# Kernel optimization log

Measured on AMD Instinct MI355X. Metric: run time of the kernel, lower is better.

Reference implementation:

```python
import jax, jax.numpy as jnp
import numpy as np

B, Q, K, D, H = 8, 200, 16384, 256, 8
ALIGN_K, CROSS_K, FF = 96, 1024, 1024
DH = D // H

def _l2norm(x):
    n = jnp.linalg.norm(x, axis=-1, keepdims=True)
    return x / jnp.maximum(n, 1e-6)

def _layernorm(x, g, b):
    mu = jnp.mean(x, axis=-1, keepdims=True)
    v = jnp.var(x, axis=-1, keepdims=True)
    return (x - mu) / jnp.sqrt(v + 1e-5) * g + b

def _mha(xq, xk, xv, in_w, in_b, out_w, out_b, bias=None):
    # torch nn.MultiheadAttention (batch_first, eval mode)
    wq, wk, wv = jnp.split(in_w, 3, axis=0)
    bq, bk, bv = jnp.split(in_b, 3, axis=0)
    def heads(x, w, bb):
        y = x @ w.T + bb
        return y.reshape(x.shape[0], x.shape[1], H, DH).transpose(0, 2, 1, 3)
    qh, kh, vh = heads(xq, wq, bq), heads(xk, wk, bk), heads(xv, wv, bv)
    s = jnp.einsum('bhqd,bhkd->bhqk', qh, kh) / (DH ** 0.5)
    if bias is not None:
        s = s + bias
    a = jax.nn.softmax(s, axis=-1)
    o = jnp.einsum('bhqk,bhkd->bhqd', a, vh).transpose(0, 2, 1, 3).reshape(xq.shape[0], xq.shape[1], D)
    return o @ out_w.T + out_b

def setup_inputs():
    key = jax.random.key(0)
    ks = jax.random.split(key, 40)
    r = lambda i, sh, s=1.0: jax.random.normal(ks[i], sh, jnp.float32) * s
    W = 0.02
    return dict(
        q=r(0, (B, Q, D)), q_pos=r(1, (B, Q, D)), memory=r(2, (B, K, D)),
        cross_attn_bias=r(3, (B, Q, K), 0.1),
        align_wq=r(4, (D, D), W), align_wm=r(5, (D, D), W),
        gate_w1=r(6, (D, 2 * D), W), gate_b1=jnp.zeros((D,), jnp.float32),
        gate_w2=r(7, (D, D), W), gate_b2=jnp.zeros((D,), jnp.float32),
        cross_wq=r(8, (D, D), W), cross_wm=r(9, (D, D), W),
        sa_in_w=r(10, (3 * D, D), W), sa_in_b=jnp.zeros((3 * D,), jnp.float32),
        sa_out_w=r(11, (D, D), W), sa_out_b=jnp.zeros((D,), jnp.float32),
        ca_in_w=r(12, (3 * D, D), W), ca_in_b=jnp.zeros((3 * D,), jnp.float32),
        ca_out_w=r(13, (D, D), W), ca_out_b=jnp.zeros((D,), jnp.float32),
        ffn_w1=r(14, (FF, D), W), ffn_b1=jnp.zeros((FF,), jnp.float32),
        ffn_w2=r(15, (D, FF), W), ffn_b2=jnp.zeros((D,), jnp.float32),
        n1_g=jnp.ones((D,), jnp.float32), n1_b=jnp.zeros((D,), jnp.float32),
        n2_g=jnp.ones((D,), jnp.float32), n2_b=jnp.zeros((D,), jnp.float32),
        n3_g=jnp.ones((D,), jnp.float32), n3_b=jnp.zeros((D,), jnp.float32))

def reference(q, q_pos, memory, cross_attn_bias, align_wq, align_wm, gate_w1, gate_b1,
              gate_w2, gate_b2, cross_wq, cross_wm, sa_in_w, sa_in_b, sa_out_w, sa_out_b,
              ca_in_w, ca_in_b, ca_out_w, ca_out_b, ffn_w1, ffn_b1, ffn_w2, ffn_b2,
              n1_g, n1_b, n2_g, n2_b, n3_g, n3_b):
    # --- query-memory align: proj+normalize+sim+topk+gather+softmax+weighted-sum ---
    qn = _l2norm(q @ align_wq.T)
    mn = _l2norm(memory @ align_wm.T)
    sim = jnp.einsum('bqd,bkd->bqk', qn, mn)            # [B,Q,K]
    vals, idx = jax.lax.top_k(sim, ALIGN_K)             # [B,Q,ALIGN_K]
    selected = jax.vmap(lambda m, i: m[i])(memory, idx) # [B,Q,ALIGN_K,D]
    w = jax.nn.softmax(vals, axis=-1)
    aligned = jnp.einsum('bqk,bqkd->bqd', w, selected)
    h = jax.nn.gelu(jnp.concatenate([q, aligned], axis=-1) @ gate_w1.T + gate_b1, approximate=False)
    gate = jax.nn.sigmoid(h @ gate_w2.T + gate_b2)
    qx = q + gate * aligned
    # --- self attention ---
    qk = qx + q_pos
    q2 = _mha(qk, qk, qx, sa_in_w, sa_in_b, sa_out_w, sa_out_b)
    qx = _layernorm(qx + q2, n1_g, n1_b)
    # --- cross-memory sparsify (topk over K) ---
    qn2 = _l2norm(qx @ cross_wq.T)
    mn2 = _l2norm(memory @ cross_wm.T)
    sim2 = jnp.einsum('bqd,bkd->bqk', qn2, mn2)
    importance = sim2.max(axis=1)                       # [B,K]
    _, kidx = jax.lax.top_k(importance, CROSS_K)        # [B,CROSS_K]
    mem_sel = jax.vmap(lambda m, i: m[i])(memory, kidx) # [B,CROSS_K,D]
    bias_sel = jnp.take_along_axis(
        cross_attn_bias, jnp.broadcast_to(kidx[:, None, :], (B, Q, CROSS_K)), axis=2)
    bias4 = jnp.broadcast_to(bias_sel[:, None], (B, H, Q, CROSS_K))
    q2 = _mha(qx + q_pos, mem_sel, mem_sel, ca_in_w, ca_in_b, ca_out_w, ca_out_b, bias4)
    qx = _layernorm(qx + q2, n2_g, n2_b)
    # --- FFN ---
    f = jax.nn.gelu(qx @ ffn_w1.T + ffn_b1, approximate=False) @ ffn_w2.T + ffn_b2
    return _layernorm(qx + f, n3_g, n3_b)
```

## Files before the change

kernel.cpp:

```cpp
#include <hip/hip_runtime.h>
#include <hip/hip_bf16.h>
#include <math.h>

#define B_ 8
#define Q_ 200
#define K_ 16384
#define D_ 256
#define H_ 8
#define DH_ 32
#define ALIGNK_ 96
#define CROSSK_ 1024
#define FF_ 1024
#define BQ_ (B_*Q_)
#define BK_ (B_*K_)

typedef unsigned short u16;
typedef short bf16x8 __attribute__((ext_vector_type(8)));
typedef float f32x4 __attribute__((ext_vector_type(4)));

__device__ __forceinline__ float b2f(u16 u){ return __uint_as_float(((unsigned)u)<<16); }
__device__ __forceinline__ u16 f2b(float f){
  unsigned x = __float_as_uint(f);
  unsigned r = x + 0x7FFFu + ((x>>16)&1u);
  return (u16)(r>>16);
}
__device__ __forceinline__ unsigned p2u(float lo, float hi){
  return (unsigned)f2b(lo) | ((unsigned)f2b(hi)<<16);
}
__device__ __forceinline__ uint4 pk8(float4 a, float4 b){
  return make_uint4(p2u(a.x,a.y), p2u(a.z,a.w), p2u(b.x,b.y), p2u(b.z,b.w));
}
__device__ __forceinline__ unsigned fkey(float f){ unsigned b=__float_as_uint(f); return (b&0x80000000u)? ~b : (b|0x80000000u); }
__device__ __forceinline__ float funkey(unsigned k){ unsigned b=(k&0x80000000u)? (k^0x80000000u) : ~k; return __uint_as_float(b); }
__device__ __forceinline__ float gelu_f(float x){ return 0.5f*x*(1.0f+erff(x*0.70710678118654752f)); }
__device__ __forceinline__ float sigmoid_f(float x){ return 1.0f/(1.0f+__expf(-x)); }

struct GArgs {
  const void* A; const void* B; const float* bias;
  float* Cf; u16* Cb; unsigned* amax;
  const int* gather;
  long lda, ldb, ldc;
  long sA, sB, sC, sAmax, sGather;
  int M, N, K, act;
};

template<int AF32, int BF32>
__global__ __launch_bounds__(256) void gemm_bt(GArgs g)
{
  const int tid = threadIdx.x;
  const int bz = blockIdx.z;
  const int m0 = blockIdx.y*64, n0 = blockIdx.x*64;
  const int lane = tid & 63, wave = tid >> 6;
  const int wr = wave >> 1, wc = wave & 1;
  __shared__ __align__(16) u16 As[64][72];
  __shared__ __align__(16) u16 Bs[64][72];
  f32x4 acc[2][2] = {};

  const int lrow = tid>>2;
  const int lk = (tid&3)*16;
  int ar = m0 + lrow; if (ar > g.M-1) ar = g.M-1;
  if (g.gather) ar = g.gather[(long)bz*g.sGather + ar];
  int br = n0 + lrow; if (br > g.N-1) br = g.N-1;
  long aoff = (long)bz*g.sA + (long)ar*g.lda + lk;
  long boff = (long)bz*g.sB + (long)br*g.ldb + lk;

  const int nk = g.K >> 6;
  for (int kt=0; kt<nk; ++kt){
    uint4 wa0, wa1, wb0, wb1;
    if (AF32){
      const float* p = (const float*)g.A + aoff;
      float4 f0 = *(const float4*)(p+0);
      float4 f1 = *(const float4*)(p+4);
      float4 f2v= *(const float4*)(p+8);
      float4 f3 = *(const float4*)(p+12);
      wa0 = pk8(f0,f1); wa1 = pk8(f2v,f3);
    } else {
      const u16* p = (const u16*)g.A + aoff;
      wa0 = *(const uint4*)p; wa1 = *(const uint4*)(p+8);
    }
    if (BF32){
      const float* p = (const float*)g.B + boff;
      float4 f0 = *(const float4*)(p+0);
      float4 f1 = *(const float4*)(p+4);
      float4 f2v= *(const float4*)(p+8);
      float4 f3 = *(const float4*)(p+12);
      wb0 = pk8(f0,f1); wb1 = pk8(f2v,f3);
    } else {
      const u16* p = (const u16*)g.B + boff;
      wb0 = *(const uint4*)p; wb1 = *(const uint4*)(p+8);
    }
    aoff += 64; boff += 64;
    __syncthreads();
    *(uint4*)&As[lrow][lk]   = wa0; *(uint4*)&As[lrow][lk+8] = wa1;
    *(uint4*)&Bs[lrow][lk]   = wb0; *(uint4*)&Bs[lrow][lk+8] = wb1;
    __syncthreads();
    #pragma unroll
    for (int kk=0; kk<2; ++kk){
      const int ko = kk*32 + (lane>>4)*8;
      bf16x8 af0 = *(const bf16x8*)&As[wr*32      + (lane&15)][ko];
      bf16x8 af1 = *(const bf16x8*)&As[wr*32 + 16 + (lane&15)][ko];
      bf16x8 bf0 = *(const bf16x8*)&Bs[wc*32      + (lane&15)][ko];
      bf16x8 bf1 = *(const bf16x8*)&Bs[wc*32 + 16 + (lane&15)][ko];
      acc[0][0] = __builtin_amdgcn_mfma_f32_16x16x32_bf16(af0, bf0, acc[0][0], 0,0,0);
      acc[0][1] = __builtin_amdgcn_mfma_f32_16x16x32_bf16(af0, bf1, acc[0][1], 0,0,0);
      acc[1][0] = __builtin_amdgcn_mfma_f32_16x16x32_bf16(af1, bf0, acc[1][0], 0,0,0);
      acc[1][1] = __builtin_amdgcn_mfma_f32_16x16x32_bf16(af1, bf1, acc[1][1], 0,0,0);
    }
  }

  if (g.amax){
    #pragma unroll
    for (int j=0;j<2;j++){
      float mx = -3.0e38f;
      #pragma unroll
      for (int i=0;i<2;i++)
        #pragma unroll
        for (int r=0;r<4;r++) mx = fmaxf(mx, acc[i][j][r]);
      mx = fmaxf(mx, __shfl_xor(mx, 16));
      mx = fmaxf(mx, __shfl_xor(mx, 32));
      if ((lane>>4)==0){
        int n = n0 + wc*32 + j*16 + (lane&15);
        if (n < g.N) atomicMax(&g.amax[(long)bz*g.sAmax + n], fkey(mx));
      }
    }
    return;
  }

  #pragma unroll
  for (int i=0;i<2;i++)
  #pragma unroll
  for (int j=0;j<2;j++)
  #pragma unroll
  for (int r=0;r<4;r++){
    int m = m0 + wr*32 + i*16 + (lane>>4)*4 + r;
    int n = n0 + wc*32 + j*16 + (lane&15);
    if (m < g.M && n < g.N){
      float v = acc[i][j][r];
      if (g.bias) v += g.bias[n];
      if (g.act==1) v = gelu_f(v);
      else if (g.act==2) v = sigmoid_f(v);
      long ci = (long)bz*g.sC + (long)m*g.ldc + n;
      if (g.Cf) g.Cf[ci] = v; else g.Cb[ci] = f2b(v);
    }
  }
}

__global__ void w2b_kernel(const float* w, u16* wb, int n)
{
  int i = (blockIdx.x*256 + threadIdx.x)*8;
  if (i < n){
    float4 a = *(const float4*)(w+i), b = *(const float4*)(w+i+4);
    *(uint4*)(wb+i) = pk8(a,b);
  }
}

template<int AF32>
__global__ __launch_bounds__(256) void proj_l2norm(
    const void* Ain, long lda, const u16* Wb, u16* outp, int R)
{
  __shared__ __align__(16) u16 As[64][72];
  __shared__ __align__(16) u16 Bs[64][72];
  const int tid = threadIdx.x;
  const int m0 = blockIdx.x*64;
  const int lane = tid & 63, wave = tid >> 6;
  f32x4 acc[4][4] = {};

  const int lrow = tid>>2, lk = (tid&3)*16;
  int ar = m0 + lrow; if (ar > R-1) ar = R-1;

  for (int kt=0; kt<4; ++kt){
    uint4 wa0, wa1;
    if (AF32){
      const float* p = (const float*)Ain + (long)ar*lda + kt*64 + lk;
      wa0 = pk8(*(const float4*)(p+0), *(const float4*)(p+4));
      wa1 = pk8(*(const float4*)(p+8), *(const float4*)(p+12));
    } else {
      const u16* p = (const u16*)Ain + (long)ar*lda + kt*64 + lk;
      wa0 = *(const uint4*)p; wa1 = *(const uint4*)(p+8);
    }
    #pragma unroll
    for (int nc=0; nc<4; ++nc){
      const u16* wp = Wb + (long)(nc*64 + lrow)*256 + kt*64 + lk;
      uint4 wb0 = *(const uint4*)wp;
      uint4 wb1 = *(const uint4*)(wp+8);
      __syncthreads();
      if (nc==0){ *(uint4*)&As[lrow][lk] = wa0; *(uint4*)&As[lrow][lk+8] = wa1; }
      *(uint4*)&Bs[lrow][lk] = wb0; *(uint4*)&Bs[lrow][lk+8] = wb1;
      __syncthreads();
      #pragma unroll
      for (int kk=0; kk<2; ++kk){
        const int ko = kk*32 + (lane>>4)*8;
        bf16x8 af = *(const bf16x8*)&As[wave*16 + (lane&15)][ko];
        #pragma unroll
        for (int j=0; j<4; j++){
          bf16x8 bfr = *(const bf16x8*)&Bs[j*16 + (lane&15)][ko];
          acc[nc][j] = __builtin_amdgcn_mfma_f32_16x16x32_bf16(af, bfr, acc[nc][j], 0,0,0);
        }
      }
    }
  }

  #pragma unroll
  for (int r=0;r<4;r++){
    float ssq = 0.f;
    #pragma unroll
    for (int nc=0;nc<4;nc++)
      #pragma unroll
      for (int j=0;j<4;j++) ssq += acc[nc][j][r]*acc[nc][j][r];
    ssq += __shfl_xor(ssq,1); ssq += __shfl_xor(ssq,2);
    ssq += __shfl_xor(ssq,4); ssq += __shfl_xor(ssq,8);
    float inv = 1.0f/fmaxf(sqrtf(ssq), 1e-6f);
    int row = m0 + wave*16 + (lane>>4)*4 + r;
    if (row < R){
      u16* op = outp + (long)row*256 + (lane&15);
      #pragma unroll
      for (int nc=0;nc<4;nc++)
        #pragma unroll
        for (int j=0;j<4;j++) op[nc*64 + j*16] = f2b(acc[nc][j][r]*inv);
    }
  }
}

__global__ __launch_bounds__(256) void topk_kernel(const float* inF, const unsigned* inK,
    long in_stride, int RANK, float* out_val, int* out_idx)
{
  __shared__ int red[2][4];
  __shared__ int redt[4];
  __shared__ int poss;
  int row = blockIdx.x, tid = threadIdx.x;
  unsigned kr[64];
  if (inF){
    const float4* p = (const float4*)(inF + (long)row*in_stride);
    #pragma unroll
    for (int jj=0;jj<16;jj++){
      float4 v = p[tid + jj*256];
      kr[jj*4+0]=fkey(v.x); kr[jj*4+1]=fkey(v.y); kr[jj*4+2]=fkey(v.z); kr[jj*4+3]=fkey(v.w);
    }
  } else {
    const uint4* p = (const uint4*)(inK + (long)row*in_stride);
    #pragma unroll
    for (int jj=0;jj<16;jj++){
      uint4 v = p[tid + jj*256];
      kr[jj*4+0]=v.x; kr[jj*4+1]=v.y; kr[jj*4+2]=v.z; kr[jj*4+3]=v.w;
    }
  }
  if (tid==0) poss = 0;

  unsigned u = 0; bool exact = false; int pp = 0;
  for (int bit=31; bit>=0; --bit){
    unsigned cand = u | (1u<<bit);
    int c = 0;
    #pragma unroll
    for (int j=0;j<64;j++) c += (kr[j] >= cand) ? 1 : 0;
    #pragma unroll
    for (int off=32; off; off>>=1) c += __shfl_down(c, off);
    if ((tid&63)==0) red[pp][tid>>6] = c;
    __syncthreads();
    c = red[pp][0]+red[pp][1]+red[pp][2]+red[pp][3];
    pp ^= 1;
    if (c >= RANK){
      u = cand;
      if (c == RANK){ exact = true; break; }
    }
  }

  int t = 0;
  if (!exact){
    int cgt = 0;
    #pragma unroll
    for (int j=0;j<64;j++) cgt += (kr[j] > u) ? 1 : 0;
    #pragma unroll
    for (int off=32; off; off>>=1) cgt += __shfl_down(cgt, off);
    __syncthreads();
    if ((tid&63)==0) redt[tid>>6] = cgt;
    __syncthreads();
    cgt = redt[0]+redt[1]+redt[2]+redt[3];
    int Req = RANK - cgt;
    for (int bit=13; bit>=0; --bit){
      int cand = t | (1<<bit);
      int c = 0;
      #pragma unroll
      for (int j=0;j<64;j++){
        int e = (tid<<2) + (j&3) + ((j>>2)<<10);
        c += (kr[j]==u && e < cand) ? 1 : 0;
      }
      #pragma unroll
      for (int off=32; off; off>>=1) c += __shfl_down(c, off);
      __syncthreads();
      if ((tid&63)==0) redt[tid>>6] = c;
      __syncthreads();
      c = redt[0]+redt[1]+redt[2]+redt[3];
      if (c < Req) t = cand;
    }
  }
  __syncthreads();
  #pragma unroll
  for (int j=0;j<64;j++){
    int e = (tid<<2) + (j&3) + ((j>>2)<<10);
    unsigned kk = kr[j];
    bool win = exact ? (kk >= u) : (kk > u || (kk == u && e <= t));
    if (win){
      int p2 = atomicAdd(&poss, 1);
      out_val[(long)row*RANK + p2] = funkey(kk);
      out_idx[(long)row*RANK + p2] = e;
    }
  }
}

__global__ __launch_bounds__(256) void align_combine(const float* vals, const int* idx,
    const float* memory, float* alignedv)
{
  __shared__ float w[96];
  __shared__ int id[96];
  __shared__ float reds[2];
  int row = blockIdx.x, tid = threadIdx.x;
  int b = row / 200;
  if (tid < 96){ w[tid] = vals[(long)row*96 + tid]; id[tid] = idx[(long)row*96 + tid]; }
  __syncthreads();
  if (tid < 64){
    float a = w[tid];
    float bb2 = (tid < 32) ? w[64+tid] : -3e38f;
    float m = fmaxf(a, bb2);
    #pragma unroll
    for (int off=32; off; off>>=1) m = fmaxf(m, __shfl_xor(m, off));
    if (tid==0) reds[0] = m;
  }
  __syncthreads();
  float m = reds[0];
  if (tid < 96) w[tid] = __expf(w[tid]-m);
  __syncthreads();
  if (tid < 64){
    float a = w[tid] + ((tid<32)? w[64+tid] : 0.f);
    #pragma unroll
    for (int off=32; off; off>>=1) a += __shfl_xor(a, off);
    if (tid==0) reds[1] = a;
  }
  __syncthreads();
  float invs = 1.0f/reds[1];
  float acc = 0.f;
  const float* mb = memory + (long)b*K_*D_;
  for (int k=0;k<96;k++) acc += w[k] * mb[(long)id[k]*D_ + tid];
  alignedv[(long)row*256 + tid] = acc*invs;
}

__global__ void make_cat(const float* q, const float* alignedv, u16* cat)
{
  int row = blockIdx.x, tid = threadIdx.x;
  long i = (long)row*256 + tid;
  cat[(long)row*512 + tid]       = f2b(q[i]);
  cat[(long)row*512 + 256 + tid] = f2b(alignedv[i]);
}

__global__ void combine_gate(const float* q, const float* q_pos, const float* alignedv,
    const float* gate, float* qx, u16* qx_b, u16* qk_b)
{
  int row = blockIdx.x, tid = threadIdx.x;
  long i = (long)row*256 + tid;
  float v = q[i] + gate[i]*alignedv[i];
  qx[i] = v;
  qx_b[i] = f2b(v);
  qk_b[i] = f2b(v + q_pos[i]);
}

__global__ __launch_bounds__(256) void add_ln(const float* x, const float* y,
    const float* g, const float* bb, const float* q_pos,
    float* out_f, u16* out_b, u16* out_pos_b)
{
  __shared__ float red[8];
  int row = blockIdx.x, tid = threadIdx.x;
  long i = (long)row*256 + tid;
  float t = fminf(fmaxf(x[i] + y[i], -1e6f), 1e6f);
  float s1 = t, s2 = t*t;
  #pragma unroll
  for (int off=32; off; off>>=1){ s1 += __shfl_down(s1,off); s2 += __shfl_down(s2,off); }
  if ((tid&63)==0){ red[(tid>>6)*2] = s1; red[(tid>>6)*2+1] = s2; }
  __syncthreads();
  s1 = red[0]+red[2]+red[4]+red[6];
  s2 = red[1]+red[3]+red[5]+red[7];
  float mu = s1 * (1.0f/256.0f);
  float var = fmaxf(s2 * (1.0f/256.0f) - mu*mu, 0.f);
  float rstd = rsqrtf(var + 1e-5f);
  float v = (t-mu)*rstd*g[tid] + bb[tid];
  if (out_f) out_f[i] = v;
  if (out_b) out_b[i] = f2b(v);
  if (out_pos_b) out_pos_b[i] = f2b(v + q_pos[i]);
}

__global__ void fill_u32(unsigned* p, unsigned val, int n)
{ int i = blockIdx.x*256 + threadIdx.x; if (i<n) p[i] = val; }

__global__ __launch_bounds__(256) void bias_gather2(const float* cbias, const int* kidx,
    float* biasTq)
{
  int qq = blockIdx.x, b = blockIdx.y;
  const float* src = cbias + ((long)b*200+qq)*(long)K_;
  float* dst = biasTq + ((long)b*200+qq)*CROSSK_;
  const int* kp = kidx + b*CROSSK_;
  for (int j=threadIdx.x; j<CROSSK_; j+=256) dst[j] = src[kp[j]];
}

__global__ __launch_bounds__(256) void qk_score(
    const u16* Qb, int q_stride, const u16* KVb, int kv_stride, int k_off,
    int Lk, int Jpad, const float* biasTq, float* S, float scale)
{
  __shared__ __align__(16) u16 Qs[64][40];
  __shared__ __align__(16) u16 Ks[64][40];
  const int bh = blockIdx.z, b = bh>>3, h = bh&7;
  const int q0 = blockIdx.y*64, j0 = blockIdx.x*64;
  const int tid = threadIdx.x, lane = tid&63, w = tid>>6;
  {
    int row = tid>>2, c8 = (tid&3)*8;
    int qr = q0+row; if (qr>199) qr=199;
    *(uint4*)&Qs[row][c8] = *(const uint4*)(Qb + (long)(b*200+qr)*q_stride + h*32 + c8);
    int j = j0+row;
    uint4 kv = make_uint4(0,0,0,0);
    if (j < Lk) kv = *(const uint4*)(KVb + (long)(b*Lk+j)*kv_stride + k_off + c8);
    *(uint4*)&Ks[row][c8] = kv;
  }
  __syncthreads();
  bf16x8 af = *(const bf16x8*)&Qs[w*16 + (lane&15)][(lane>>4)*8];
  f32x4 acc[4];
  #pragma unroll
  for (int jj=0;jj<4;jj++){
    f32x4 zz = {};
    bf16x8 bfr = *(const bf16x8*)&Ks[jj*16 + (lane&15)][(lane>>4)*8];
    acc[jj] = __builtin_amdgcn_mfma_f32_16x16x32_bf16(af, bfr, zz, 0,0,0);
  }
  #pragma unroll
  for (int jj=0;jj<4;jj++)
  #pragma unroll
  for (int r=0;r<4;r++){
    int q = q0 + w*16 + (lane>>4)*4 + r;
    int j = j0 + jj*16 + (lane&15);
    if (q < 200){
      float s = acc[jj][r]*scale;
      if (biasTq) s += biasTq[((long)(b*200+q))*Jpad + j];
      if (j >= Lk) s = -3e38f;
      S[((long)bh*200 + q)*Jpad + j] = s;
    }
  }
}

template<int JP>
__global__ __launch_bounds__(256) void softmax_p(const float* S, u16* P)
{
  __shared__ float red[8];
  const long base = (long)blockIdx.x * JP;
  const int tid = threadIdx.x;
  constexpr int PER = JP/256;
  float v[PER];
  float m = -3e38f;
  #pragma unroll
  for (int i=0;i<PER;i++){ v[i] = S[base + tid + i*256]; m = fmaxf(m, v[i]); }
  #pragma unroll
  for (int off=32; off; off>>=1) m = fmaxf(m, __shfl_xor(m, off));
  if ((tid&63)==0) red[tid>>6] = m;
  __syncthreads();
  m = fmaxf(fmaxf(red[0],red[1]), fmaxf(red[2],red[3]));
  float s = 0.f;
  #pragma unroll
  for (int i=0;i<PER;i++){ v[i] = __expf(v[i]-m); s += v[i]; }
  #pragma unroll
  for (int off=32; off; off>>=1) s += __shfl_xor(s, off);
  if ((tid&63)==0) red[4+(tid>>6)] = s;
  __syncthreads();
  s = red[4]+red[5]+red[6]+red[7];
  float inv = 1.0f/s;
  #pragma unroll
  for (int i=0;i<PER;i++) P[base + tid + i*256] = f2b(v[i]*inv);
}

__global__ __launch_bounds__(256) void pv_kernel(
    const u16* P, int Jpad, const u16* KVb, int kv_stride, int v_off, int Lk,
    u16* outp)
{
  __shared__ __align__(16) u16 Vt[32][72];
  const int bh = blockIdx.y, b = bh>>3, h = bh&7;
  const int q0 = blockIdx.x*64;
  const int tid = threadIdx.x, lane = tid&63, w = tid>>6;
  f32x4 acc[2] = {};
  int qa = q0 + w*16 + (lane&15); if (qa>199) qa=199;
  const u16* Prow = P + ((long)bh*200 + qa)*Jpad;
  const int jrow = lane;
  const int d0 = w*8;

  for (int j0=0; j0<Jpad; j0+=64){
    int j = j0 + jrow;
    uint4 vv = make_uint4(0,0,0,0);
    if (j < Lk) vv = *(const uint4*)(KVb + (long)(b*Lk+j)*kv_stride + v_off + d0);
    __syncthreads();
    Vt[d0+0][jrow] = (u16)(vv.x&0xffffu); Vt[d0+1][jrow] = (u16)(vv.x>>16);
    Vt[d0+2][jrow] = (u16)(vv.y&0xffffu); Vt[d0+3][jrow] = (u16)(vv.y>>16);
    Vt[d0+4][jrow] = (u16)(vv.z&0xffffu); Vt[d0+5][jrow] = (u16)(vv.z>>16);
    Vt[d0+6][jrow] = (u16)(vv.w&0xffffu); Vt[d0+7][jrow] = (u16)(vv.w>>16);
    __syncthreads();
    #pragma unroll
    for (int ks=0; ks<2; ks++){
      bf16x8 af = *(const bf16x8*)(Prow + j0 + ks*32 + (lane>>4)*8);
      #pragma unroll
      for (int dd=0; dd<2; dd++){
        bf16x8 bfr = *(const bf16x8*)&Vt[dd*16 + (lane&15)][ks*32 + (lane>>4)*8];
        acc[dd] = __builtin_amdgcn_mfma_f32_16x16x32_bf16(af, bfr, acc[dd], 0,0,0);
      }
    }
  }
  #pragma unroll
  for (int dd=0; dd<2; dd++)
  #pragma unroll
  for (int r=0; r<4; r++){
    int qq = q0 + w*16 + (lane>>4)*4 + r;
    if (qq < 200)
      outp[((long)(b*200+qq))*256 + h*32 + dd*16 + (lane&15)] = f2b(acc[dd][r]);
  }
}

__global__ __launch_bounds__(256) void attn_kernel(
    const u16* Qb, int q_stride,
    const u16* KVb, int kv_stride, int k_off, int v_off, int Lk,
    const float* biasTq,
    int nsplit, int chunk,
    float* opart, float* mlpart, float scale)
{
  __shared__ float Ks[64][36];
  __shared__ float Vs[64][36];
  const int b = blockIdx.z, h = blockIdx.y;
  const int split = blockIdx.x % nsplit;
  const int q0 = (blockIdx.x / nsplit) * 64;
  const int tid = threadIdx.x;
  const int cg = tid & 3, r = tid >> 2;
  const int kbeg = split*chunk;
  int kend = kbeg + chunk; if (kend > Lk) kend = Lk;

  int qr = q0 + r; if (qr > 199) qr = 199;
  float qreg[32];
  {
    const u16* qp = Qb + (long)(b*200+qr)*q_stride + h*32;
    #pragma unroll
    for (int w=0; w<4; w++){
      uint4 u = *(const uint4*)(qp + w*8);
      qreg[w*8+0]=b2f((u16)(u.x&0xffffu))*scale; qreg[w*8+1]=b2f((u16)(u.x>>16))*scale;
      qreg[w*8+2]=b2f((u16)(u.y&0xffffu))*scale; qreg[w*8+3]=b2f((u16)(u.y>>16))*scale;
      qreg[w*8+4]=b2f((u16)(u.z&0xffffu))*scale; qreg[w*8+5]=b2f((u16)(u.z>>16))*scale;
      qreg[w*8+6]=b2f((u16)(u.w&0xffffu))*scale; qreg[w*8+7]=b2f((u16)(u.w>>16))*scale;
    }
  }
  const float* bT = biasTq ? biasTq + ((long)(b*200+qr))*CROSSK_ : nullptr;

  float o32[32];
  #pragma unroll
  for (int i=0;i<32;i++) o32[i]=0.f;
  float mrun = -3e38f, lrun = 0.f;

  const int srow = tid>>2, sc8 = (tid&3)*8;
  for (int j0=kbeg; j0<kend; j0+=64){
    int kr = j0 + srow; if (kr > kend-1) kr = kend-1;
    const long base = (long)(b*Lk + kr)*kv_stride;
    uint4 ku = *(const uint4*)(KVb + base + k_off + sc8);
    uint4 vu = *(const uint4*)(KVb + base + v_off + sc8);
    __syncthreads();
    {
      float4 f0, f1;
      f0.x=b2f((u16)(ku.x&0xffffu)); f0.y=b2f((u16)(ku.x>>16)); f0.z=b2f((u16)(ku.y&0xffffu)); f0.w=b2f((u16)(ku.y>>16));
      f1.x=b2f((u16)(ku.z&0xffffu)); f1.y=b2f((u16)(ku.z>>16)); f1.z=b2f((u16)(ku.w&0xffffu)); f1.w=b2f((u16)(ku.w>>16));
      *(float4*)&Ks[srow][sc8] = f0; *(float4*)&Ks[srow][sc8+4] = f1;
      f0.x=b2f((u16)(vu.x&0xffffu)); f0.y=b2f((u16)(vu.x>>16)); f0.z=b2f((u16)(vu.y&0xffffu)); f0.w=b2f((u16)(vu.y>>16));
      f1.x=b2f((u16)(vu.z&0xffffu)); f1.y=b2f((u16)(vu.z>>16)); f1.z=b2f((u16)(vu.w&0xffffu)); f1.w=b2f((u16)(vu.w>>16));
      *(float4*)&Vs[srow][sc8] = f0; *(float4*)&Vs[srow][sc8+4] = f1;
    }
    __syncthreads();

    float sv[16];
    float mloc = -3e38f;
    #pragma unroll
    for (int jj=0;jj<16;jj++){
      const int c = cg + jj*4;
      const float4* kp = (const float4*)&Ks[c][0];
      float a = 0.f;
      #pragma unroll
      for (int dq=0;dq<8;dq++){
        float4 kv = kp[dq];
        a += qreg[dq*4+0]*kv.x + qreg[dq*4+1]*kv.y + qreg[dq*4+2]*kv.z + qreg[dq*4+3]*kv.w;
      }
      if (bT) a += bT[j0 + c];
      if (j0 + c >= kend) a = -3e38f;
      sv[jj] = a; mloc = fmaxf(mloc, a);
    }
    mloc = fmaxf(mloc, __shfl_xor(mloc,1));
    mloc = fmaxf(mloc, __shfl_xor(mloc,2));
    const float mnew = fmaxf(mrun, mloc);
    const float alpha = __expf(mrun - mnew);
    float lloc = 0.f;
    #pragma unroll
    for (int jj=0;jj<16;jj++){
      float p = (j0 + cg + jj*4 >= kend) ? 0.f : __expf(sv[jj]-mnew);
      sv[jj] = p; lloc += p;
    }
    lloc += __shfl_xor(lloc,1);
    lloc += __shfl_xor(lloc,2);
    lrun = lrun*alpha + lloc;
    #pragma unroll
    for (int i=0;i<32;i++) o32[i] *= alpha;
    #pragma unroll
    for (int jj=0;jj<16;jj++){
      const int c = cg + jj*4;
      const float p = sv[jj];
      const float4* vp = (const float4*)&Vs[c][0];
      #pragma unroll
      for (int dq=0;dq<8;dq++){
        float4 v = vp[dq];
        o32[dq*4+0] += p*v.x; o32[dq*4+1] += p*v.y; o32[dq*4+2] += p*v.z; o32[dq*4+3] += p*v.w;
      }
    }
    mrun = mnew;
  }

  #pragma unroll
  for (int d=0;d<32;d++){
    float v = o32[d];
    v += __shfl_xor(v,1);
    v += __shfl_xor(v,2);
    o32[d] = v;
  }
  if (q0 + r < 200){
    const long pbase = (((long)(b*H_+h)*nsplit + split)*200) + (q0 + r);
    float* op = opart + pbase*32;
    #pragma unroll
    for (int i=0;i<8;i++) op[cg*8+i] = o32[cg*8+i];
    if (cg==0){ mlpart[pbase*2] = mrun; mlpart[pbase*2+1] = lrun; }
  }
}

__global__ __launch_bounds__(256) void attn_combine(const float* opart, const float* mlpart,
    int nsplit, u16* outp)
{
  int row = blockIdx.x;
  int b = row/200, qi = row%200;
  int tid = threadIdx.x;
  int h = tid>>5, d = tid&31;
  const long base = ((long)(b*H_+h)*nsplit)*200 + qi;
  float M = -3e38f;
  for (int s=0;s<nsplit;s++) M = fmaxf(M, mlpart[(base + (long)s*200)*2]);
  float L = 0.f, acc = 0.f;
  for (int s=0;s<nsplit;s++){
    const long ix = base + (long)s*200;
    float w = __expf(mlpart[ix*2] - M);
    L   += mlpart[ix*2+1]*w;
    acc += opart[ix*32 + d]*w;
  }
  outp[(long)row*256 + h*32 + d] = f2b(acc / fmaxf(L, 1e-30f));
}

extern "C" void kernel_launch(void* const* d_in, const int* in_sizes, int n_in,
                              void* d_out, int out_size, void* d_ws, size_t ws_size,
                              hipStream_t stream)
{
  const float* q        = (const float*)d_in[0];
  const float* q_pos    = (const float*)d_in[1];
  const float* memory   = (const float*)d_in[2];
  const float* cbias    = (const float*)d_in[3];
  const float* align_wq = (const float*)d_in[4];
  const float* align_wm = (const float*)d_in[5];
  const float* gate_w1  = (const float*)d_in[6];
  const float* gate_b1  = (const float*)d_in[7];
  const float* gate_w2  = (const float*)d_in[8];
  const float* gate_b2  = (const float*)d_in[9];
  const float* cross_wq = (const float*)d_in[10];
  const float* cross_wm = (const float*)d_in[11];
  const float* sa_in_w  = (const float*)d_in[12];
  const float* sa_in_b  = (const float*)d_in[13];
  const float* sa_out_w = (const float*)d_in[14];
  const float* sa_out_b = (const float*)d_in[15];
  const float* ca_in_w  = (const float*)d_in[16];
  const float* ca_in_b  = (const float*)d_in[17];
  const float* ca_out_w = (const float*)d_in[18];
  const float* ca_out_b = (const float*)d_in[19];
  const float* ffn_w1   = (const float*)d_in[20];
  const float* ffn_b1   = (const float*)d_in[21];
  const float* ffn_w2   = (const float*)d_in[22];
  const float* ffn_b2   = (const float*)d_in[23];
  const float* n1_g = (const float*)d_in[24];
  const float* n1_b = (const float*)d_in[25];
  const float* n2_g = (const float*)d_in[26];
  const float* n2_b = (const float*)d_in[27];
  const float* n3_g = (const float*)d_in[28];
  const float* n3_b = (const float*)d_in[29];
  float* out = (float*)d_out;

  char* wsb = (char*)d_ws;
  size_t off = 0;
  auto alloc = [&](size_t bytes)->char*{
    char* p = wsb + off; off = (off + bytes + 255) & ~(size_t)255; return p;
  };
  const int NSPLIT = 4;
  u16*    qn_bf   = (u16*)   alloc((size_t)BQ_*D_*2);
  float*  vals96  = (float*) alloc((size_t)BQ_*96*4);
  int*    idx96   = (int*)   alloc((size_t)BQ_*96*4);
  float*  alignedv= (float*) alloc((size_t)BQ_*D_*4);
  u16*    cat_bf  = (u16*)   alloc((size_t)BQ_*512*2);
  u16*    h_bf    = (u16*)   alloc((size_t)BQ_*D_*2);
  float*  gatebuf = (float*) alloc((size_t)BQ_*D_*4);
  float*  qx      = (float*) alloc((size_t)BQ_*D_*4);
  u16*    qx_bf   = (u16*)   alloc((size_t)BQ_*D_*2);
  u16*    qk_bf   = (u16*)   alloc((size_t)BQ_*D_*2);
  u16*    qpos2_bf= (u16*)   alloc((size_t)BQ_*D_*2);
  u16*    qkv_bf  = (u16*)   alloc((size_t)BQ_*768*2);
  u16*    attO_bf = (u16*)   alloc((size_t)BQ_*D_*2);
  float*  q2      = (float*) alloc((size_t)BQ_*D_*4);
  unsigned* imp   = (unsigned*)alloc((size_t)B_*K_*4);
  int*    kidx    = (int*)   alloc((size_t)B_*CROSSK_*4);
  u16*    cq_bf   = (u16*)   alloc((size_t)BQ_*D_*2);
  u16*    f1_bf   = (u16*)   alloc((size_t)BQ_*FF_*2);
  float*  f2buf   = (float*) alloc((size_t)BQ_*D_*4);
  float*  opart   = (float*) alloc((size_t)B_*H_*NSPLIT*200*32*4);
  float*  mlpart  = (float*) alloc((size_t)B_*H_*NSPLIT*200*2*4);
  float*  biasTq  = (float*) alloc((size_t)B_*Q_*CROSSK_*4);
  u16*    wb_alwq = (u16*)   alloc((size_t)D_*D_*2);
  u16*    wb_alwm = (u16*)   alloc((size_t)D_*D_*2);
  u16*    wb_crwq = (u16*)   alloc((size_t)D_*D_*2);
  u16*    wb_crwm = (u16*)   alloc((size_t)D_*D_*2);

  const size_t kv_bytes   = (size_t)B_*CROSSK_*512*2;
  const size_t mn_full    = (size_t)BK_*D_*2;
  const size_t mn_small   = (size_t)K_*D_*2;
  const size_t sim_full   = (size_t)BQ_*K_*4;
  size_t remain = (ws_size > off) ? ws_size - off : 0;
  bool fullws = remain >= mn_full + sim_full + (1u<<20);
  size_t mn_bytes = fullws ? mn_full : (mn_small > kv_bytes ? mn_small : kv_bytes);
  int simRows;
  if (fullws) simRows = BQ_;
  else {
    size_t left = (remain > mn_bytes + (1u<<18)) ? remain - mn_bytes - (1u<<18) : 0;
    long r = (long)(left / ((size_t)K_*4));
    simRows = (int)(r < 8 ? 8 : (r > Q_ ? Q_ : r));
  }
  u16*   mn_bf  = (u16*)  alloc(mn_bytes);
  u16*   kvbuf  = (u16*)  mn_bf;
  float* simbuf = (float*)alloc((size_t)simRows*K_*4);
  float* Sbuf = simbuf;
  u16*   Pbuf = (u16*)(simbuf + (size_t)64*200*1024);

  auto gemm = [&](int af32, int bf32,
                  const void* A, long lda, long sA,
                  const void* Bm, long ldb, long sB,
                  int M, int N, int Kd,
                  const float* bias, int act,
                  float* Cf, u16* Cb, long ldc, long sC,
                  unsigned* amax, long sAmax,
                  const int* gather, long sGather, int Z){
    GArgs ga;
    ga.A=A; ga.B=Bm; ga.bias=bias; ga.Cf=Cf; ga.Cb=Cb; ga.amax=amax; ga.gather=gather;
    ga.lda=lda; ga.ldb=ldb; ga.ldc=ldc; ga.sA=sA; ga.sB=sB; ga.sC=sC;
    ga.sAmax=sAmax; ga.sGather=sGather;
    ga.M=M; ga.N=N; ga.K=Kd; ga.act=act;
    dim3 grid(N/64, (M+63)/64, Z);
    if (af32 && bf32)      gemm_bt<1,1><<<grid, 256, 0, stream>>>(ga);
    else if (af32)         gemm_bt<1,0><<<grid, 256, 0, stream>>>(ga);
    else if (bf32)         gemm_bt<0,1><<<grid, 256, 0, stream>>>(ga);
    else                   gemm_bt<0,0><<<grid, 256, 0, stream>>>(ga);
  };
  const float ascale = 0.17677669529663687f;

  w2b_kernel<<<32,256,0,stream>>>(align_wq, wb_alwq, D_*D_);
  w2b_kernel<<<32,256,0,stream>>>(align_wm, wb_alwm, D_*D_);
  w2b_kernel<<<32,256,0,stream>>>(cross_wq, wb_crwq, D_*D_);
  w2b_kernel<<<32,256,0,stream>>>(cross_wm, wb_crwm, D_*D_);

  proj_l2norm<1><<<BQ_/64,256,0,stream>>>(q, 256, wb_alwq, qn_bf, BQ_);
  if (fullws){
    proj_l2norm<1><<<BK_/64,256,0,stream>>>(memory, 256, wb_alwm, mn_bf, BK_);
    gemm(0,0, qn_bf,256,(long)200*256, mn_bf,256,(long)K_*256, 200,K_,256,
         nullptr,0, simbuf,nullptr,K_,(long)200*K_, nullptr,0, nullptr,0, B_);
    topk_kernel<<<BQ_,256,0,stream>>>(simbuf, nullptr, K_, 96, vals96, idx96);
  } else {
    for (int b=0;b<B_;b++){
      proj_l2norm<1><<<K_/64,256,0,stream>>>(memory + (size_t)b*K_*256, 256, wb_alwm, mn_bf, K_);
      for (int q0=0; q0<Q_; q0+=simRows){
        int rows = (Q_ - q0 < simRows) ? (Q_ - q0) : simRows;
        gemm(0,0, qn_bf + ((size_t)b*200+q0)*256,256,0, mn_bf,256,0, rows,K_,256,
             nullptr,0, simbuf,nullptr,K_,0, nullptr,0, nullptr,0, 1);
        topk_kernel<<<rows,256,0,stream>>>(simbuf, nullptr, K_, 96,
             vals96 + ((size_t)b*200+q0)*96, idx96 + ((size_t)b*200+q0)*96);
      }
    }
  }
  align_combine<<<BQ_,256,0,stream>>>(vals96, idx96, memory, alignedv);

  make_cat<<<BQ_,256,0,stream>>>(q, alignedv, cat_bf);
  gemm(0,1, cat_bf,512,0, gate_w1,512,0, BQ_,256,512, gate_b1,1, nullptr,h_bf,256,0, nullptr,0, nullptr,0, 1);
  gemm(0,1, h_bf,256,0, gate_w2,256,0, BQ_,256,256, gate_b2,2, gatebuf,nullptr,256,0, nullptr,0, nullptr,0, 1);
  combine_gate<<<BQ_,256,0,stream>>>(q, q_pos, alignedv, gatebuf, qx, qx_bf, qk_bf);

  gemm(0,1, qk_bf,256,0, sa_in_w,256,0, BQ_,512,256, sa_in_b,0, nullptr,qkv_bf,768,0, nullptr,0, nullptr,0, 1);
  gemm(0,1, qx_bf,256,0, sa_in_w+512*256,256,0, BQ_,256,256, sa_in_b+512,0, nullptr,qkv_bf+512,768,0, nullptr,0, nullptr,0, 1);
  if (fullws){
    qk_score<<<dim3(256/64, 4, B_*H_),256,0,stream>>>(qkv_bf,768, qkv_bf,768,256,
        200, 256, nullptr, Sbuf, ascale);
    softmax_p<256><<<B_*H_*200,256,0,stream>>>(Sbuf, Pbuf);
    pv_kernel<<<dim3(4, B_*H_),256,0,stream>>>(Pbuf, 256, qkv_bf,768,512, 200, attO_bf);
  } else {
    attn_kernel<<<dim3(4*NSPLIT,H_,B_),256,0,stream>>>(qkv_bf,768, qkv_bf,768,256,512,200,
        nullptr, NSPLIT,64, opart,mlpart, ascale);
    attn_combine<<<BQ_,256,0,stream>>>(opart, mlpart, NSPLIT, attO_bf);
  }
  gemm(0,1, attO_bf,256,0, sa_out_w,256,0, BQ_,256,256, sa_out_b,0, q2,nullptr,256,0, nullptr,0, nullptr,0, 1);
  add_ln<<<BQ_,256,0,stream>>>(qx, q2, n1_g, n1_b, q_pos, qx, qx_bf, qpos2_bf);

  proj_l2norm<0><<<BQ_/64,256,0,stream>>>(qx_bf, 256, wb_crwq, qn_bf, BQ_);
  fill_u32<<<(B_*K_+255)/256,256,0,stream>>>(imp, 0u, B_*K_);
  if (fullws){
    proj_l2norm<1><<<BK_/64,256,0,stream>>>(memory, 256, wb_crwm, mn_bf, BK_);
    gemm(0,0, qn_bf,256,(long)200*256, mn_bf,256,(long)K_*256, 200,K_,256,
         nullptr,0, nullptr,nullptr,0,0, imp,(long)K_, nullptr,0, B_);
  } else {
    for (int b=0;b<B_;b++){
      proj_l2norm<1><<<K_/64,256,0,stream>>>(memory + (size_t)b*K_*256, 256, wb_crwm, mn_bf, K_);
      gemm(0,0, qn_bf + (size_t)b*200*256,256,0, mn_bf,256,0, 200,K_,256,
           nullptr,0, nullptr,nullptr,0,0, imp + (size_t)b*K_,(long)K_, nullptr,0, 1);
    }
  }
  topk_kernel<<<B_,256,0,stream>>>(nullptr, imp, K_, CROSSK_, vals96 , kidx);

  bias_gather2<<<dim3(Q_, B_),256,0,stream>>>(cbias, kidx, biasTq);
  gemm(1,1, memory,256,(long)K_*256, ca_in_w+256*256,256,0, CROSSK_,512,256,
       ca_in_b+256,0, nullptr,kvbuf,512,(long)CROSSK_*512, nullptr,0, kidx,(long)CROSSK_, B_);
  gemm(0,1, qpos2_bf,256,0, ca_in_w,256,0, BQ_,256,256, ca_in_b,0, nullptr,cq_bf,256,0, nullptr,0, nullptr,0, 1);
  if (fullws){
    qk_score<<<dim3(CROSSK_/64, 4, B_*H_),256,0,stream>>>(cq_bf,256, kvbuf,512,0,
        CROSSK_, CROSSK_, biasTq, Sbuf, ascale);
    softmax_p<1024><<<B_*H_*200,256,0,stream>>>(Sbuf, Pbuf);
    pv_kernel<<<dim3(4, B_*H_),256,0,stream>>>(Pbuf, CROSSK_, kvbuf,512,256, CROSSK_, attO_bf);
  } else {
    attn_kernel<<<dim3(4*NSPLIT,H_,B_),256,0,stream>>>(cq_bf,256, kvbuf,512,0,256,CROSSK_,
        biasTq, NSPLIT,256, opart,mlpart, ascale);
    attn_combine<<<BQ_,256,0,stream>>>(opart, mlpart, NSPLIT, attO_bf);
  }
  gemm(0,1, attO_bf,256,0, ca_out_w,256,0, BQ_,256,256, ca_out_b,0, q2,nullptr,256,0, nullptr,0, nullptr,0, 1);
  add_ln<<<BQ_,256,0,stream>>>(qx, q2, n2_g, n2_b, nullptr, qx, qx_bf, nullptr);

  gemm(0,1, qx_bf,256,0, ffn_w1,256,0, BQ_,FF_,256, ffn_b1,1, nullptr,f1_bf,FF_,0, nullptr,0, nullptr,0, 1);
  gemm(0,1, f1_bf,FF_,0, ffn_w2,FF_,0, BQ_,256,FF_, ffn_b2,0, f2buf,nullptr,256,0, nullptr,0, nullptr,0, 1);
  add_ln<<<BQ_,256,0,stream>>>(qx, f2buf, n3_g, n3_b, nullptr, out, nullptr, nullptr);

  (void)in_sizes; (void)n_in; (void)out_size;
}
```

Before: 938.5 us.

## Replace block-wide radix top-k with per-wave select then single-wave merge

Adds a specialised top-96 kernel for the alignment similarity rows. Each wave radix-selects a local threshold over its 4096 keys using only shuffles, so the per-bit block barriers are gone. It then writes up to 160 candidates per wave to shared memory, and a single wave does a second radix select on 46-bit keys (value plus index tiebreak) to pick the final 96. The aim is to cut barrier and shared-memory reduction cost per bit. The risk is candidate truncation if ties push a wave past its cap, and the final merge being serialised on one wave.

```diff
diff --git a/kernel.cpp b/kernel.cpp
--- a/kernel.cpp
+++ b/kernel.cpp
@@ -15,6 +15,7 @@
 #define BK_ (B_*K_)
 
 typedef unsigned short u16;
+typedef unsigned long long u64;
 typedef short bf16x8 __attribute__((ext_vector_type(8)));
 typedef float f32x4 __attribute__((ext_vector_type(4)));
 
@@ -217,6 +218,95 @@
       for (int nc=0;nc<4;nc++)
         #pragma unroll
         for (int j=0;j<4;j++) op[nc*64 + j*16] = f2b(acc[nc][j][r]*inv);
+    }
+  }
+}
+
+#define CAP_ 160
+__global__ __launch_bounds__(256) void topk96_kernel(const float* inF,
+    float* out_val, int* out_idx)
+{
+  __shared__ u64 cand[4*CAP_];
+  __shared__ int cnum[4];
+  __shared__ int poss;
+  const int row = blockIdx.x, tid = threadIdx.x;
+  const int lane = tid & 63, w = tid >> 6;
+  if (tid < 4) cnum[tid] = 0;
+  if (tid == 0) poss = 0;
+
+  unsigned kr[64];
+  {
+    const float4* p = (const float4*)(inF + (long)row*K_);
+    #pragma unroll
+    for (int jj=0;jj<16;jj++){
+      float4 v = p[tid + jj*256];
+      kr[jj*4+0]=fkey(v.x); kr[jj*4+1]=fkey(v.y); kr[jj*4+2]=fkey(v.z); kr[jj*4+3]=fkey(v.w);
+    }
+  }
+
+  unsigned u = 0;
+  for (int bit=31; bit>=0; --bit){
+    unsigned cv = u | (1u<<bit);
+    int c = 0;
+    #pragma unroll
+    for (int j=0;j<64;j++) c += (kr[j] >= cv) ? 1 : 0;
+    #pragma unroll
+    for (int off=32; off; off>>=1) c += __shfl_xor(c, off);
+    if (c >= 96){
+      u = cv;
+      if (c == 96) break;
+    }
+  }
+  __syncthreads();
+  #pragma unroll
+  for (int j=0;j<64;j++){
+    if (kr[j] >= u){
+      int e = (tid<<2) + (j&3) + ((j>>2)<<10);
+      int s = atomicAdd(&cnum[w], 1);
+      if (s < CAP_) cand[w*CAP_ + s] = ((u64)kr[j] << 14) | (u64)(unsigned)(16383 - e);
+    }
+  }
+  __syncthreads();
+
+  if (w == 0){
+    int n0 = cnum[0]; if (n0 > CAP_) n0 = CAP_;
+    int n1 = cnum[1]; if (n1 > CAP_) n1 = CAP_;
+    int n2 = cnum[2]; if (n2 > CAP_) n2 = CAP_;
+    int n3 = cnum[3]; if (n3 > CAP_) n3 = CAP_;
+    const int tot = n0+n1+n2+n3;
+    u64 ck[10];
+    #pragma unroll
+    for (int t=0;t<10;t++){
+      int g = lane + t*64;
+      u64 v = 0;
+      if (g < n0)                 v = cand[g];
+      else if (g < n0+n1)         v = cand[CAP_   + g-n0];
+      else if (g < n0+n1+n2)      v = cand[2*CAP_ + g-n0-n1];
+      else if (g < tot)           v = cand[3*CAP_ + g-n0-n1-n2];
+      ck[t] = v;
+    }
+    u64 U = 0;
+    for (int bit=45; bit>=0; --bit){
+      u64 cv = U | (1ull<<bit);
+      int c = 0;
+      #pragma unroll
+      for (int t=0;t<10;t++) c += (ck[t] >= cv) ? 1 : 0;
+      #pragma unroll
+      for (int off=32; off; off>>=1) c += __shfl_xor(c, off);
+      if (c >= 96){
+        U = cv;
+        if (c == 96) break;
+      }
+    }
+    #pragma unroll
+    for (int t=0;t<10;t++){
+      if (ck[t] >= U && ck[t] != 0){
+        int s = atomicAdd(&poss, 1);
+        unsigned kk = (unsigned)(ck[t] >> 14);
+        int idx = 16383 - (int)(ck[t] & 0x3FFFull);
+        out_val[(long)row*96 + s] = funkey(kk);
+        out_idx[(long)row*96 + s] = idx;
+      }
     }
   }
 }
@@ -770,7 +860,7 @@
     proj_l2norm<1><<<BK_/64,256,0,stream>>>(memory, 256, wb_alwm, mn_bf, BK_);
     gemm(0,0, qn_bf,256,(long)200*256, mn_bf,256,(long)K_*256, 200,K_,256,
          nullptr,0, simbuf,nullptr,K_,(long)200*K_, nullptr,0, nullptr,0, B_);
-    topk_kernel<<<BQ_,256,0,stream>>>(simbuf, nullptr, K_, 96, vals96, idx96);
+    topk96_kernel<<<BQ_,256,0,stream>>>(simbuf, vals96, idx96);
   } else {
     for (int b=0;b<B_;b++){
       proj_l2norm<1><<<K_/64,256,0,stream>>>(memory + (size_t)b*K_*256, 256, wb_alwm, mn_bf, K_);
@@ -778,7 +868,7 @@
         int rows = (Q_ - q0 < simRows) ? (Q_ - q0) : simRows;
         gemm(0,0, qn_bf + ((size_t)b*200+q0)*256,256,0, mn_bf,256,0, rows,K_,256,
              nullptr,0, simbuf,nullptr,K_,0, nullptr,0, nullptr,0, 1);
-        topk_kernel<<<rows,256,0,stream>>>(simbuf, nullptr, K_, 96,
+        topk96_kernel<<<rows,256,0,stream>>>(simbuf,
              vals96 + ((size_t)b*200+q0)*96, idx96 + ((size_t)b*200+q0)*96);
       }
     }
```

After: 874.1 us. 1.07x faster.
